# Kernel optimization log

Measured on AMD Instinct MI355X. Metric: run time of the kernel, lower is better.

## Reference

```python
import jax, jax.numpy as jnp
import numpy as np

B, Q, D = 4, 8192, 256
L, P = 2, 8
H0 = W0 = 128
H1 = W1 = 64
EPS = 1e-5


def _bilinear_sample(feat, gx, gy):
    """grid_sample bilinear, padding_mode='border', align_corners=False.
    feat: (B, D, H, W); gx, gy: (B, N) in [-1, 1]. Returns (B, N, D)."""
    b, d, h, w = feat.shape
    # unnormalize (align_corners=False)
    x = ((gx + 1.0) * w - 1.0) * 0.5
    y = ((gy + 1.0) * h - 1.0) * 0.5
    # border padding: clamp coords into valid range
    x = jnp.clip(x, 0.0, w - 1.0)
    y = jnp.clip(y, 0.0, h - 1.0)
    x0 = jnp.floor(x)
    y0 = jnp.floor(y)
    wx = x - x0
    wy = y - y0
    x0i = x0.astype(jnp.int32)
    y0i = y0.astype(jnp.int32)
    x1i = jnp.minimum(x0i + 1, w - 1)
    y1i = jnp.minimum(y0i + 1, h - 1)
    fhw = feat.reshape(b, d, h * w)  # (B, D, H*W)

    def gather(iy, ix):
        idx = iy * w + ix  # (B, N)
        return jnp.take_along_axis(fhw, idx[:, None, :], axis=2)  # (B, D, N)

    v00 = gather(y0i, x0i)
    v01 = gather(y0i, x1i)
    v10 = gather(y1i, x0i)
    v11 = gather(y1i, x1i)
    wxb = wx[:, None, :]
    wyb = wy[:, None, :]
    top = v00 * (1.0 - wxb) + v01 * wxb
    bot = v10 * (1.0 - wxb) + v11 * wxb
    out = top * (1.0 - wyb) + bot * wyb  # (B, D, N)
    return out.transpose(0, 2, 1)  # (B, N, D)


def setup_inputs() -> dict:
    key = jax.random.key(0)
    ks = jax.random.split(key, 12)
    s = 0.02
    return {
        "q": jax.random.normal(ks[0], (B, Q, D), jnp.float32),
        "map0": jax.random.normal(ks[1], (B, D, H0, W0), jnp.float32),
        "map1": jax.random.normal(ks[2], (B, D, H1, W1), jnp.float32),
        "base_ref": jax.random.uniform(ks[3], (B, L, 2), jnp.float32),
        "Wrd": jax.random.normal(ks[4], (D, L * 2), jnp.float32) * s,
        "brd": jax.random.normal(ks[5], (L * 2,), jnp.float32) * s,
        "Woff": jax.random.normal(ks[6], (D, L * P * 2), jnp.float32) * s,
        "boff": jax.random.normal(ks[7], (L * P * 2,), jnp.float32) * 1.5,
        "Wattn": jax.random.normal(ks[8], (D, L * P), jnp.float32) * s,
        "battn": jax.random.normal(ks[9], (L * P,), jnp.float32) * s,
        "Wout": jax.random.normal(ks[10], (D, D), jnp.float32) * s,
        "bout": jax.random.normal(ks[11], (D,), jnp.float32) * s,
    }


def reference(q, map0, map1, base_ref, Wrd, brd, Woff, boff, Wattn, battn, Wout, bout):
    b, qn, d = q.shape
    maps = [map0, map1]
    # per-level reference points, refined through inverse-sigmoid space
    base = jnp.clip(base_ref, EPS, 1.0 - EPS)[:, None, :, :]  # (B, 1, L, 2)
    logit_base = jnp.log(base / (1.0 - base))
    ref_delta = (q @ Wrd + brd).reshape(b, qn, L, 2)
    ref = jax.nn.sigmoid(logit_base + ref_delta)  # (B, Q, L, 2)
    offsets = (q @ Woff + boff).reshape(b, qn, L, P, 2)
    attn_logits = (q @ Wattn + battn).reshape(b, qn, L * P)
    attn = jax.nn.softmax(attn_logits, axis=-1).reshape(b, qn, L, P)

    out = jnp.zeros((b, qn, d), jnp.float32)
    for level, feat in enumerate(maps):
        h, w = feat.shape[2], feat.shape[3]
        normalizer = jnp.array([w, h], jnp.float32)
        loc = ref[:, :, level, None, :] + offsets[:, :, level] / normalizer  # (B,Q,P,2)
        if level == 1:
            loc = jnp.stack([loc[..., 0], jnp.remainder(loc[..., 1], 1.0)], axis=-1)
        loc = loc * 2.0 - 1.0
        gx = loc[..., 0].reshape(b, qn * P)
        gy = loc[..., 1].reshape(b, qn * P)
        samp = _bilinear_sample(feat, gx, gy).reshape(b, qn, P, d)
        out = out + jnp.sum(samp * attn[:, :, level, :, None], axis=2)
    return out @ Wout + bout
```

## Files before the change

### kernel.cpp

```cpp
#include <hip/hip_runtime.h>
#include <hip/hip_bf16.h>

#define BQ 4
#define QN 8192
#define DD 256
#define LL 2
#define PP 8
#define H0c 128
#define W0c 128
#define H1c 64
#define W1c 64
#define NCP 64
#define EPSF 1e-5f

typedef __attribute__((ext_vector_type(8))) short short8;
typedef __attribute__((ext_vector_type(4))) float floatx4;

static __device__ __forceinline__ float bf2f(unsigned short u) {
    union { unsigned int u; float f; } x;
    x.u = ((unsigned int)u) << 16;
    return x.f;
}
static __device__ __forceinline__ unsigned short f2bf(float f) {
    __hip_bfloat16 h = __float2bfloat16(f);
    return __builtin_bit_cast(unsigned short, h);
}

__global__ __launch_bounds__(256) void transpose_cast(const float* __restrict__ in,
                                                      __hip_bfloat16* __restrict__ out,
                                                      int HW) {
    __shared__ float tile[32][33];
    int b   = blockIdx.z;
    int hw0 = blockIdx.x * 32;
    int c0  = blockIdx.y * 32;
    const float* inb = in + (size_t)b * DD * HW;
    __hip_bfloat16* outb = out + (size_t)b * DD * HW;
    int tx = threadIdx.x, ty = threadIdx.y;
#pragma unroll
    for (int j = 0; j < 32; j += 8)
        tile[ty + j][tx] = inb[(size_t)(c0 + ty + j) * HW + hw0 + tx];
    __syncthreads();
#pragma unroll
    for (int j = 0; j < 32; j += 8)
        outb[(size_t)(hw0 + ty + j) * DD + c0 + tx] = __float2bfloat16(tile[tx][ty + j]);
}

__global__ __launch_bounds__(256) void pack_wall(const float* __restrict__ Wrd, const float* __restrict__ brd,
                                                 const float* __restrict__ Woff, const float* __restrict__ boff,
                                                 const float* __restrict__ Wattn, const float* __restrict__ battn,
                                                 float* __restrict__ Wall, float* __restrict__ bias64) {
    int idx = blockIdx.x * 256 + threadIdx.x;
    int k = idx >> 6, c = idx & 63;
    float v = (c < 4)  ? Wrd[k * 4 + c]
            : (c < 36) ? Woff[k * 32 + (c - 4)]
            : (c < 52) ? Wattn[k * 16 + (c - 36)]
            : 0.f;
    Wall[idx] = v;
    if (idx < 64) {
        float bv = (idx < 4)  ? brd[idx]
                 : (idx < 36) ? boff[idx - 4]
                 : (idx < 52) ? battn[idx - 36]
                 : 0.f;
        bias64[idx] = bv;
    }
}

__global__ __launch_bounds__(256) void proj_gemm(const float* __restrict__ q,
                                                 const float* __restrict__ Wall,
                                                 const float* __restrict__ bias64,
                                                 float* __restrict__ proj) {
    __shared__ float As[32][68];
    __shared__ float Bs[32][64];
    int tid = threadIdx.x;
    int tx = tid & 15, ty = tid >> 4;
    int m0 = blockIdx.x * 64;
    float acc[4][4] = {};

    for (int kt = 0; kt < DD; kt += 32) {
#pragma unroll
        for (int j = 0; j < 8; j++) {
            int e = tid + 256 * j;
            int r = e >> 5, k = e & 31;
            As[k][r] = q[(size_t)(m0 + r) * DD + kt + k];
        }
#pragma unroll
        for (int j = 0; j < 2; j++) {
            int e = tid + 256 * j;
            int k = e >> 6, nn = e & 63;
            Bs[kt ? 0 : 0][0] = Bs[0][0];
            Bs[k + j * 0][nn] = Wall[(size_t)(kt + k) * 64 + nn];
        }
#pragma unroll
        for (int j = 2; j < 8; j++) {
            int e = tid + 256 * j;
            int k = e >> 6, nn = e & 63;
            Bs[k][nn] = Wall[(size_t)(kt + k) * 64 + nn];
        }
        __syncthreads();
#pragma unroll
        for (int k = 0; k < 32; k++) {
            const float4 a4 = *(const float4*)&As[k][ty * 4];
            const float4 b4 = *(const float4*)&Bs[k][tx * 4];
            acc[0][0] += a4.x * b4.x; acc[0][1] += a4.x * b4.y; acc[0][2] += a4.x * b4.z; acc[0][3] += a4.x * b4.w;
            acc[1][0] += a4.y * b4.x; acc[1][1] += a4.y * b4.y; acc[1][2] += a4.y * b4.z; acc[1][3] += a4.y * b4.w;
            acc[2][0] += a4.z * b4.x; acc[2][1] += a4.z * b4.y; acc[2][2] += a4.z * b4.z; acc[2][3] += a4.z * b4.w;
            acc[3][0] += a4.w * b4.x; acc[3][1] += a4.w * b4.y; acc[3][2] += a4.w * b4.z; acc[3][3] += a4.w * b4.w;
        }
        __syncthreads();
    }

    float4 bias = *(const float4*)&bias64[tx * 4];
#pragma unroll
    for (int i = 0; i < 4; i++) {
        int m = m0 + ty * 4 + i;
        float4 v;
        v.x = acc[i][0] + bias.x;
        v.y = acc[i][1] + bias.y;
        v.z = acc[i][2] + bias.z;
        v.w = acc[i][3] + bias.w;
        *(float4*)&proj[(size_t)m * NCP + tx * 4] = v;
    }
}

__global__ __launch_bounds__(256) void sample_kernel(const unsigned short* __restrict__ mapT0,
                                                     const unsigned short* __restrict__ mapT1,
                                                     const float* __restrict__ proj,
                                                     const float* __restrict__ base_ref,
                                                     unsigned short* __restrict__ S) {
    __shared__ float pr[4][64];
    __shared__ int   si[4][16][4];
    __shared__ float sw[4][16][4];
    int n0  = blockIdx.x * 4;
    int tid = threadIdx.x;
    int ql  = tid >> 6;
    int lx  = tid & 63;

    pr[ql][lx] = proj[(size_t)(n0 + ql) * NCP + lx];
    __syncthreads();

    if (tid < 64) {
        int qq = tid >> 4, s = tid & 15, l = s >> 3;
        int n = n0 + qq, b = n >> 13;
        const float* p = pr[qq];
        float mx = p[36];
#pragma unroll
        for (int i = 1; i < 16; i++) mx = fmaxf(mx, p[36 + i]);
        float sum = 0.f;
#pragma unroll
        for (int i = 0; i < 16; i++) sum += __expf(p[36 + i] - mx);
        float a = __expf(p[36 + s] - mx) / sum;

        int W = l ? W1c : W0c;
        int H = l ? H1c : H0c;
        float Wf = (float)W, Hf = (float)H;

        float bx = base_ref[(b * LL + l) * 2 + 0];
        float by = base_ref[(b * LL + l) * 2 + 1];
        bx = fminf(fmaxf(bx, EPSF), 1.f - EPSF);
        by = fminf(fmaxf(by, EPSF), 1.f - EPSF);
        float lgx = logf(bx / (1.f - bx));
        float lgy = logf(by / (1.f - by));
        float refx = 1.f / (1.f + __expf(-(lgx + p[l * 2 + 0])));
        float refy = 1.f / (1.f + __expf(-(lgy + p[l * 2 + 1])));

        float locx = refx + p[4 + s * 2 + 0] / Wf;
        float locy = refy + p[4 + s * 2 + 1] / Hf;
        if (l == 1) locy = locy - floorf(locy);

        float gx = locx * 2.f - 1.f;
        float gy = locy * 2.f - 1.f;
        float x = ((gx + 1.f) * Wf - 1.f) * 0.5f;
        float y = ((gy + 1.f) * Hf - 1.f) * 0.5f;
        x = fminf(fmaxf(x, 0.f), Wf - 1.f);
        y = fminf(fmaxf(y, 0.f), Hf - 1.f);
        float x0f = floorf(x), y0f = floorf(y);
        float wx = x - x0f, wy = y - y0f;
        int x0 = (int)x0f, y0 = (int)y0f;
        int x1 = min(x0 + 1, W - 1);
        int y1 = min(y0 + 1, H - 1);
        int rowb = b * H * W;
        si[qq][s][0] = ((rowb + y0 * W) + x0) * DD;
        si[qq][s][1] = ((rowb + y0 * W) + x1) * DD;
        si[qq][s][2] = ((rowb + y1 * W) + x0) * DD;
        si[qq][s][3] = ((rowb + y1 * W) + x1) * DD;
        float omx = 1.f - wx, omy = 1.f - wy;
        sw[qq][s][0] = a * omx * omy;
        sw[qq][s][1] = a * wx  * omy;
        sw[qq][s][2] = a * omx * wy;
        sw[qq][s][3] = a * wx  * wy;
    }
    __syncthreads();

    int c4 = lx * 4;
    float acc0 = 0.f, acc1 = 0.f, acc2 = 0.f, acc3 = 0.f;
#pragma unroll
    for (int s = 0; s < 16; s++) {
        const unsigned short* m = (s < 8) ? mapT0 : mapT1;
        int i0 = si[ql][s][0], i1 = si[ql][s][1], i2 = si[ql][s][2], i3 = si[ql][s][3];
        float w00 = sw[ql][s][0], w01 = sw[ql][s][1], w10 = sw[ql][s][2], w11 = sw[ql][s][3];
        ushort4 u00 = *(const ushort4*)(m + i0 + c4);
        ushort4 u01 = *(const ushort4*)(m + i1 + c4);
        ushort4 u10 = *(const ushort4*)(m + i2 + c4);
        ushort4 u11 = *(const ushort4*)(m + i3 + c4);
        acc0 += w00 * bf2f(u00.x) + w01 * bf2f(u01.x) + w10 * bf2f(u10.x) + w11 * bf2f(u11.x);
        acc1 += w00 * bf2f(u00.y) + w01 * bf2f(u01.y) + w10 * bf2f(u10.y) + w11 * bf2f(u11.y);
        acc2 += w00 * bf2f(u00.z) + w01 * bf2f(u01.z) + w10 * bf2f(u10.z) + w11 * bf2f(u11.z);
        acc3 += w00 * bf2f(u00.w) + w01 * bf2f(u01.w) + w10 * bf2f(u10.w) + w11 * bf2f(u11.w);
    }
    ushort4 o;
    o.x = f2bf(acc0); o.y = f2bf(acc1); o.z = f2bf(acc2); o.w = f2bf(acc3);
    *(ushort4*)(S + (size_t)(n0 + ql) * DD + c4) = o;
}

__global__ __launch_bounds__(256) void out_mfma(const unsigned short* __restrict__ S,
                                                const unsigned short* __restrict__ WT,
                                                const float* __restrict__ bout,
                                                float* __restrict__ out) {
    int wave = threadIdx.x >> 6, lane = threadIdx.x & 63;
    int m0 = blockIdx.x * 64 + wave * 16;
    int mrow = lane & 15, quad = lane >> 4;
    const unsigned short* Sp = S + (size_t)(m0 + mrow) * DD + quad * 8;

    floatx4 acc[16];
#pragma unroll
    for (int nt = 0; nt < 16; nt++) acc[nt] = {0.f, 0.f, 0.f, 0.f};

    for (int k0 = 0; k0 < DD; k0 += 32) {
        short8 a = *(const short8*)(Sp + k0);
#pragma unroll
        for (int nt = 0; nt < 16; nt++) {
            short8 b = *(const short8*)(WT + (size_t)(nt * 16 + mrow) * DD + k0 + quad * 8);
            acc[nt] = __builtin_amdgcn_mfma_f32_16x16x32_bf16(a, b, acc[nt], 0, 0, 0);
        }
    }

    int rbase = quad * 4;
#pragma unroll
    for (int nt = 0; nt < 16; nt++) {
        float bv = bout[nt * 16 + mrow];
#pragma unroll
        for (int r = 0; r < 4; r++) {
            out[(size_t)(m0 + rbase + r) * DD + nt * 16 + mrow] = acc[nt][r] + bv;
        }
    }
}

extern "C" void kernel_launch(void* const* d_in, const int* in_sizes, int n_in,
                              void* d_out, int out_size, void* d_ws, size_t ws_size,
                              hipStream_t stream) {
    const float* q        = (const float*)d_in[0];
    const float* map0     = (const float*)d_in[1];
    const float* map1     = (const float*)d_in[2];
    const float* base_ref = (const float*)d_in[3];
    const float* Wrd      = (const float*)d_in[4];
    const float* brd      = (const float*)d_in[5];
    const float* Woff     = (const float*)d_in[6];
    const float* boff     = (const float*)d_in[7];
    const float* Wattn    = (const float*)d_in[8];
    const float* battn    = (const float*)d_in[9];
    const float* Wout     = (const float*)d_in[10];
    const float* bout     = (const float*)d_in[11];
    float* out = (float*)d_out;

    char* ws = (char*)d_ws;
    __hip_bfloat16* mapT0  = (__hip_bfloat16*)(ws + 0);
    __hip_bfloat16* mapT1  = (__hip_bfloat16*)(ws + 33554432);
    __hip_bfloat16* WoutT  = (__hip_bfloat16*)(ws + 41943040);
    float*          Wall   = (float*)(ws + 42074112);
    float*          bias64 = (float*)(ws + 42139648);
    float*          proj   = (float*)(ws + 42139904);
    unsigned short* Sbuf   = (unsigned short*)(ws + 50528512);

    transpose_cast<<<dim3(H0c * W0c / 32, DD / 32, BQ), dim3(32, 8), 0, stream>>>(map0, mapT0, H0c * W0c);
    transpose_cast<<<dim3(H1c * W1c / 32, DD / 32, BQ), dim3(32, 8), 0, stream>>>(map1, mapT1, H1c * W1c);
    transpose_cast<<<dim3(DD / 32, DD / 32, 1), dim3(32, 8), 0, stream>>>(Wout, WoutT, DD);

    pack_wall<<<dim3(64), dim3(256), 0, stream>>>(Wrd, brd, Woff, boff, Wattn, battn, Wall, bias64);

    proj_gemm<<<dim3(BQ * QN / 64), dim3(256), 0, stream>>>(q, Wall, bias64, proj);

    sample_kernel<<<dim3(BQ * QN / 4), dim3(256), 0, stream>>>(
        (const unsigned short*)mapT0, (const unsigned short*)mapT1, proj, base_ref, Sbuf);

    out_mfma<<<dim3(BQ * QN / 64), dim3(256), 0, stream>>>(
        Sbuf, (const unsigned short*)WoutT, bout, out);
}
```

Baseline: 289.0 us.

## Move sampling-descriptor computation into projection GEMM and stream compact descriptors

The softmax, reference-point refinement and bilinear index/weight computation move from the sampling kernel into the projection GEMM epilogue, which now writes compact per-sample descriptors: a base offset with packed dx/dy deltas plus fp16 corner weights. The sampling kernel no longer stages through shared memory or calls __syncthreads, and it no longer serialises on a single wave computing the descriptors. Each wave reads its descriptors directly and issues the gathers. The cost is fp16 rounding of the attention-bilinear weights and an extra global round trip for the descriptors, in place of the fp32 projection output.

```diff
diff --git a/kernel.cpp b/kernel.cpp
--- a/kernel.cpp
+++ b/kernel.cpp
@@ -5,16 +5,16 @@
 #define QN 8192
 #define DD 256
 #define LL 2
-#define PP 8
 #define H0c 128
 #define W0c 128
 #define H1c 64
 #define W1c 64
-#define NCP 64
 #define EPSF 1e-5f
 
+typedef unsigned short ushort_t;
 typedef __attribute__((ext_vector_type(8))) short short8;
 typedef __attribute__((ext_vector_type(4))) float floatx4;
+typedef __attribute__((ext_vector_type(4))) _Float16 half4;
 
 static __device__ __forceinline__ float bf2f(unsigned short u) {
     union { unsigned int u; float f; } x;
@@ -65,12 +65,15 @@
     }
 }
 
-__global__ __launch_bounds__(256) void proj_gemm(const float* __restrict__ q,
+__global__ __launch_bounds__(256) void proj_desc(const float* __restrict__ q,
                                                  const float* __restrict__ Wall,
                                                  const float* __restrict__ bias64,
-                                                 float* __restrict__ proj) {
+                                                 const float* __restrict__ base_ref,
+                                                 int2* __restrict__ dsi,
+                                                 half4* __restrict__ dsw) {
     __shared__ float As[32][68];
     __shared__ float Bs[32][64];
+    __shared__ float prs[64][68];
     int tid = threadIdx.x;
     int tx = tid & 15, ty = tid >> 4;
     int m0 = blockIdx.x * 64;
@@ -84,14 +87,7 @@
             As[k][r] = q[(size_t)(m0 + r) * DD + kt + k];
         }
 #pragma unroll
-        for (int j = 0; j < 2; j++) {
-            int e = tid + 256 * j;
-            int k = e >> 6, nn = e & 63;
-            Bs[kt ? 0 : 0][0] = Bs[0][0];
-            Bs[k + j * 0][nn] = Wall[(size_t)(kt + k) * 64 + nn];
-        }
-#pragma unroll
-        for (int j = 2; j < 8; j++) {
+        for (int j = 0; j < 8; j++) {
             int e = tid + 256 * j;
             int k = e >> 6, nn = e & 63;
             Bs[k][nn] = Wall[(size_t)(kt + k) * 64 + nn];
@@ -112,43 +108,32 @@
     float4 bias = *(const float4*)&bias64[tx * 4];
 #pragma unroll
     for (int i = 0; i < 4; i++) {
-        int m = m0 + ty * 4 + i;
         float4 v;
         v.x = acc[i][0] + bias.x;
         v.y = acc[i][1] + bias.y;
         v.z = acc[i][2] + bias.z;
         v.w = acc[i][3] + bias.w;
-        *(float4*)&proj[(size_t)m * NCP + tx * 4] = v;
-    }
-}
-
-__global__ __launch_bounds__(256) void sample_kernel(const unsigned short* __restrict__ mapT0,
-                                                     const unsigned short* __restrict__ mapT1,
-                                                     const float* __restrict__ proj,
-                                                     const float* __restrict__ base_ref,
-                                                     unsigned short* __restrict__ S) {
-    __shared__ float pr[4][64];
-    __shared__ int   si[4][16][4];
-    __shared__ float sw[4][16][4];
-    int n0  = blockIdx.x * 4;
-    int tid = threadIdx.x;
-    int ql  = tid >> 6;
-    int lx  = tid & 63;
-
-    pr[ql][lx] = proj[(size_t)(n0 + ql) * NCP + lx];
+        *(float4*)&prs[ty * 4 + i][tx * 4] = v;
+    }
     __syncthreads();
 
-    if (tid < 64) {
-        int qq = tid >> 4, s = tid & 15, l = s >> 3;
-        int n = n0 + qq, b = n >> 13;
-        const float* p = pr[qq];
-        float mx = p[36];
-#pragma unroll
-        for (int i = 1; i < 16; i++) mx = fmaxf(mx, p[36 + i]);
-        float sum = 0.f;
-#pragma unroll
-        for (int i = 0; i < 16; i++) sum += __expf(p[36 + i] - mx);
-        float a = __expf(p[36 + s] - mx) / sum;
+    int ql = tid >> 2, sq = tid & 3;
+    int n = m0 + ql, b = n >> 13;
+    const float* p = prs[ql];
+
+    float mx = p[36];
+#pragma unroll
+    for (int i = 1; i < 16; i++) mx = fmaxf(mx, p[36 + i]);
+    float sum = 0.f;
+#pragma unroll
+    for (int i = 0; i < 16; i++) sum += __expf(p[36 + i] - mx);
+    float inv = 1.f / sum;
+
+#pragma unroll
+    for (int u = 0; u < 4; u++) {
+        int s = sq * 4 + u;
+        int l = s >> 3;
+        float a = __expf(p[36 + s] - mx) * inv;
 
         int W = l ? W1c : W0c;
         int H = l ? H1c : H0c;
@@ -176,50 +161,67 @@
         float x0f = floorf(x), y0f = floorf(y);
         float wx = x - x0f, wy = y - y0f;
         int x0 = (int)x0f, y0 = (int)y0f;
-        int x1 = min(x0 + 1, W - 1);
-        int y1 = min(y0 + 1, H - 1);
-        int rowb = b * H * W;
-        si[qq][s][0] = ((rowb + y0 * W) + x0) * DD;
-        si[qq][s][1] = ((rowb + y0 * W) + x1) * DD;
-        si[qq][s][2] = ((rowb + y1 * W) + x0) * DD;
-        si[qq][s][3] = ((rowb + y1 * W) + x1) * DD;
+        unsigned int dx = (x0 + 1 <= W - 1) ? DD : 0;
+        unsigned int dy = (y0 + 1 <= H - 1) ? (unsigned)(W * DD) : 0;
+        int base = ((b * H + y0) * W + x0) * DD;
+
         float omx = 1.f - wx, omy = 1.f - wy;
-        sw[qq][s][0] = a * omx * omy;
-        sw[qq][s][1] = a * wx  * omy;
-        sw[qq][s][2] = a * omx * wy;
-        sw[qq][s][3] = a * wx  * wy;
-    }
-    __syncthreads();
-
+        half4 w;
+        w[0] = (_Float16)(a * omx * omy);
+        w[1] = (_Float16)(a * wx  * omy);
+        w[2] = (_Float16)(a * omx * wy);
+        w[3] = (_Float16)(a * wx  * wy);
+
+        dsi[(size_t)n * 16 + s] = make_int2(base, (int)((dy << 16) | dx));
+        dsw[(size_t)n * 16 + s] = w;
+    }
+}
+
+__global__ __launch_bounds__(256) void sample_kernel(const ushort_t* __restrict__ mapT0,
+                                                     const ushort_t* __restrict__ mapT1,
+                                                     const int2* __restrict__ dsi,
+                                                     const half4* __restrict__ dsw,
+                                                     ushort_t* __restrict__ S) {
+    int tid = threadIdx.x;
+    int qw = __builtin_amdgcn_readfirstlane(tid >> 6);
+    int lx = tid & 63;
+    int n = blockIdx.x * 4 + qw;
     int c4 = lx * 4;
-    float acc0 = 0.f, acc1 = 0.f, acc2 = 0.f, acc3 = 0.f;
+    const int2*  gi = dsi + (size_t)n * 16;
+    const half4* gw = dsw + (size_t)n * 16;
+
+    float a0 = 0.f, a1 = 0.f, a2 = 0.f, a3 = 0.f;
 #pragma unroll
     for (int s = 0; s < 16; s++) {
-        const unsigned short* m = (s < 8) ? mapT0 : mapT1;
-        int i0 = si[ql][s][0], i1 = si[ql][s][1], i2 = si[ql][s][2], i3 = si[ql][s][3];
-        float w00 = sw[ql][s][0], w01 = sw[ql][s][1], w10 = sw[ql][s][2], w11 = sw[ql][s][3];
-        ushort4 u00 = *(const ushort4*)(m + i0 + c4);
-        ushort4 u01 = *(const ushort4*)(m + i1 + c4);
-        ushort4 u10 = *(const ushort4*)(m + i2 + c4);
-        ushort4 u11 = *(const ushort4*)(m + i3 + c4);
-        acc0 += w00 * bf2f(u00.x) + w01 * bf2f(u01.x) + w10 * bf2f(u10.x) + w11 * bf2f(u11.x);
-        acc1 += w00 * bf2f(u00.y) + w01 * bf2f(u01.y) + w10 * bf2f(u10.y) + w11 * bf2f(u11.y);
-        acc2 += w00 * bf2f(u00.z) + w01 * bf2f(u01.z) + w10 * bf2f(u10.z) + w11 * bf2f(u11.z);
-        acc3 += w00 * bf2f(u00.w) + w01 * bf2f(u01.w) + w10 * bf2f(u10.w) + w11 * bf2f(u11.w);
+        int2 g = gi[s];
+        half4 wh = gw[s];
+        const ushort_t* mp = (s < 8) ? mapT0 : mapT1;
+        int dx = g.y & 0xffff;
+        int dy = (int)(((unsigned int)g.y) >> 16);
+        const ushort_t* p0 = mp + g.x + c4;
+        ushort4 u00 = *(const ushort4*)(p0);
+        ushort4 u01 = *(const ushort4*)(p0 + dx);
+        ushort4 u10 = *(const ushort4*)(p0 + dy);
+        ushort4 u11 = *(const ushort4*)(p0 + dx + dy);
+        float w00 = (float)wh[0], w01 = (float)wh[1], w10 = (float)wh[2], w11 = (float)wh[3];
+        a0 += w00 * bf2f(u00.x) + w01 * bf2f(u01.x) + w10 * bf2f(u10.x) + w11 * bf2f(u11.x);
+        a1 += w00 * bf2f(u00.y) + w01 * bf2f(u01.y) + w10 * bf2f(u10.y) + w11 * bf2f(u11.y);
+        a2 += w00 * bf2f(u00.z) + w01 * bf2f(u01.z) + w10 * bf2f(u10.z) + w11 * bf2f(u11.z);
+        a3 += w00 * bf2f(u00.w) + w01 * bf2f(u01.w) + w10 * bf2f(u10.w) + w11 * bf2f(u11.w);
     }
     ushort4 o;
-    o.x = f2bf(acc0); o.y = f2bf(acc1); o.z = f2bf(acc2); o.w = f2bf(acc3);
-    *(ushort4*)(S + (size_t)(n0 + ql) * DD + c4) = o;
-}
-
-__global__ __launch_bounds__(256) void out_mfma(const unsigned short* __restrict__ S,
-                                                const unsigned short* __restrict__ WT,
+    o.x = f2bf(a0); o.y = f2bf(a1); o.z = f2bf(a2); o.w = f2bf(a3);
+    *(ushort4*)(S + (size_t)n * DD + c4) = o;
+}
+
+__global__ __launch_bounds__(256) void out_mfma(const ushort_t* __restrict__ S,
+                                                const ushort_t* __restrict__ WT,
                                                 const float* __restrict__ bout,
                                                 float* __restrict__ out) {
     int wave = threadIdx.x >> 6, lane = threadIdx.x & 63;
     int m0 = blockIdx.x * 64 + wave * 16;
     int mrow = lane & 15, quad = lane >> 4;
-    const unsigned short* Sp = S + (size_t)(m0 + mrow) * DD + quad * 8;
+    const ushort_t* Sp = S + (size_t)(m0 + mrow) * DD + quad * 8;
 
     floatx4 acc[16];
 #pragma unroll
@@ -268,8 +270,9 @@
     __hip_bfloat16* WoutT  = (__hip_bfloat16*)(ws + 41943040);
     float*          Wall   = (float*)(ws + 42074112);
     float*          bias64 = (float*)(ws + 42139648);
-    float*          proj   = (float*)(ws + 42139904);
-    unsigned short* Sbuf   = (unsigned short*)(ws + 50528512);
+    int2*           dsi    = (int2*)(ws + 42139904);
+    half4*          dsw    = (half4*)(ws + 46334208);
+    ushort_t*       Sbuf   = (ushort_t*)(ws + 50528512);
 
     transpose_cast<<<dim3(H0c * W0c / 32, DD / 32, BQ), dim3(32, 8), 0, stream>>>(map0, mapT0, H0c * W0c);
     transpose_cast<<<dim3(H1c * W1c / 32, DD / 32, BQ), dim3(32, 8), 0, stream>>>(map1, mapT1, H1c * W1c);
@@ -277,11 +280,11 @@
 
     pack_wall<<<dim3(64), dim3(256), 0, stream>>>(Wrd, brd, Woff, boff, Wattn, battn, Wall, bias64);
 
-    proj_gemm<<<dim3(BQ * QN / 64), dim3(256), 0, stream>>>(q, Wall, bias64, proj);
+    proj_desc<<<dim3(BQ * QN / 64), dim3(256), 0, stream>>>(q, Wall, bias64, base_ref, dsi, dsw);
 
     sample_kernel<<<dim3(BQ * QN / 4), dim3(256), 0, stream>>>(
-        (const unsigned short*)mapT0, (const unsigned short*)mapT1, proj, base_ref, Sbuf);
+        (const ushort_t*)mapT0, (const ushort_t*)mapT1, dsi, dsw, Sbuf);
 
     out_mfma<<<dim3(BQ * QN / 64), dim3(256), 0, stream>>>(
-        Sbuf, (const unsigned short*)WoutT, bout, out);
-}
+        Sbuf, (const ushort_t*)WoutT, bout, out);
+}
```

Measured after the change: 289.9 us. Within noise of the previous version (+0.3%).
